# Performance work log

Hardware: AMD Instinct MI355X
Metric: run time of the kernel (lower is better)

The kernel has to match this reference:

```python
import jax, jax.numpy as jnp
import numpy as np

GAMMA = 0.9
TEMPERATURE = 0.07
BASE_TEMPERATURE = 0.07
U_SIZE = 15_000_000
BSZ, N_VIEWS, DIM = 2048, 2, 256


def setup_inputs() -> dict:
    key = jax.random.key(0)
    kf, = jax.random.split(key, 1)
    feats = jax.random.normal(kf, (BSZ, N_VIEWS, DIM), dtype=jnp.float32)
    # contrastive features are unit-normalized in practice
    feats = feats / jnp.linalg.norm(feats, axis=-1, keepdims=True)
    index = jnp.arange(BSZ, dtype=jnp.int64) if jax.config.jax_enable_x64 else jnp.arange(BSZ, dtype=jnp.int32)
    u = jnp.zeros((U_SIZE, 1), dtype=jnp.float32)
    return {"index": index, "features": feats, "u": u}


def reference(index, features, u):
    B, V, D = features.shape          # bsz, n_views, dim
    N = B * V
    eye_b = jnp.eye(B, dtype=jnp.float32)

    # torch.cat(torch.unbind(features, dim=1), dim=0) -> [V*B, D], views stacked
    contrast_feature = jnp.transpose(features, (1, 0, 2)).reshape(N, D)
    anchor_feature = contrast_feature  # contrast_mode == 'all'

    # [N, N] similarity logits
    anchor_dot_contrast = jnp.matmul(anchor_feature, contrast_feature.T) / TEMPERATURE
    logits_max = jax.lax.stop_gradient(jnp.max(anchor_dot_contrast, axis=1, keepdims=True))
    logits = anchor_dot_contrast - logits_max

    # positive mask: tiled identity with self-contrast removed
    mask = jnp.tile(eye_b, (V, V))
    logits_mask = 1.0 - jnp.eye(N, dtype=jnp.float32)  # scatter of zeros on the diagonal
    pos_mask = mask * logits_mask
    neg_mask = 1.0 - pos_mask

    # detached negative exp-logits (EMA statistics)
    neg_exp_logits = jax.lax.stop_gradient(jnp.exp(logits) * neg_mask)

    # indexed EMA buffer update: u[index] = (1-g)*u[index] + g*rowsum[:B]
    row_sum = jnp.sum(neg_exp_logits, axis=1, keepdims=True)[:B]   # [B, 1]
    u_new = (1.0 - GAMMA) * u[index] + GAMMA * row_sum             # [B, 1]
    # (buffer write: u = u.at[index].set(u_new); only u_new is read below)

    p_neg_pairs = neg_exp_logits / jnp.tile(u_new, (V, 1))         # [N, N], detached numer/denom
    log_prob = logits - jnp.sum(p_neg_pairs * logits * neg_mask, axis=1, keepdims=True)

    mean_log_prob_pos = jnp.sum(pos_mask * log_prob, axis=1) / jnp.sum(pos_mask, axis=1)
    loss = -(TEMPERATURE / BASE_TEMPERATURE) * mean_log_prob_pos
    return loss.reshape(V, B).mean()
```

## Files before the change

kernel.cpp:

```cpp
#include <hip/hip_runtime.h>


#define BSZ   2048
#define NROW  4096
#define DDIM  256
#define NB64  64
#define NT2   (NB64 * (NB64 + 1) / 2)
#define C1    (1.4426950408889634f / 0.07f)
#define LN2   0.6931471805599453f

typedef __attribute__((ext_vector_type(8))) __bf16 bf16x8;
typedef __attribute__((ext_vector_type(4))) float f32x4;

__device__ __forceinline__ short f2bs(float x) {
    __bf16 b = (__bf16)x;
    return __builtin_bit_cast(short, b);
}

__device__ __forceinline__ const float* crow_ptr(const float* feats, int i) {
    return feats + (((i & (BSZ - 1)) * 2 + (i >> 11)) << 8);
}

__global__ __launch_bounds__(256) void prep_kernel(const float* __restrict__ feats,
        float* __restrict__ msd, float* __restrict__ EWzero,
        short* __restrict__ CmF) {
    int tid = threadIdx.x;
    int z = blockIdx.x * 256 + tid;
    if (z < 2 * NROW) EWzero[z] = 0.0f;

    int lane = tid & 63;
    int row  = (blockIdx.x << 2) + (tid >> 6);
    const float4* src = (const float4*)crow_ptr(feats, row);
    float4 v = src[lane];
    float a0 = (float)(__bf16)v.x, a1 = (float)(__bf16)v.y;
    float a2 = (float)(__bf16)v.z, a3 = (float)(__bf16)v.w;
    float s = a0 * a0 + a1 * a1 + a2 * a2 + a3 * a3;
    #pragma unroll
    for (int off = 32; off; off >>= 1) s += __shfl_xor(s, off, 64);
    if (lane == 0) msd[row] = -s * C1;

    int gid  = z;
    int quad = gid & 3;
    int l15  = (gid >> 2) & 15;
    int rt   = (gid >> 6) & 3;
    int k    = (gid >> 8) & 7;
    int b    = gid >> 12;
    int srow = (b << 6) + (rt << 4) + l15;
    int kel  = (k << 5) + (quad << 3);
    const float4* fp = (const float4*)(crow_ptr(feats, srow) + kel);
    float4 v0 = fp[0], v1 = fp[1];
    short h[8] = { f2bs(v0.x), f2bs(v0.y), f2bs(v0.z), f2bs(v0.w),
                   f2bs(v1.x), f2bs(v1.y), f2bs(v1.z), f2bs(v1.w) };
    *(int4*)(CmF + gid * 8) = *(int4*)h;
}

__global__ __launch_bounds__(64, 2) void gemm_sym(const short* __restrict__ CmF,
        const float* __restrict__ msd, float* __restrict__ E,
        float* __restrict__ W2, float* __restrict__ Lpos) {
    int lane = threadIdx.x;
    int quad = lane >> 4;
    int l15  = lane & 15;

    int t = blockIdx.x;
    int p = (int)((sqrtf(8.0f * (float)t + 1.0f) - 1.0f) * 0.5f);
    while ((p + 1) * (p + 2) / 2 <= t) ++p;
    while (p * (p + 1) / 2 > t) --p;
    int q = t - p * (p + 1) / 2;
    int rowBase = q << 6;
    int colBase = p << 6;
    bool offdiag = (p != q);

    const short* aB = CmF + q * 16384 + ((l15 << 2) + quad) * 8;
    const short* bB = CmF + p * 16384 + ((l15 << 2) + quad) * 8;

    f32x4 acc[4][4];
    #pragma unroll
    for (int a = 0; a < 4; ++a)
        #pragma unroll
        for (int c = 0; c < 4; ++c) acc[a][c] = (f32x4){0.f, 0.f, 0.f, 0.f};

    bf16x8 aF[3][4], bF[3][4];
    #pragma unroll
    for (int rt = 0; rt < 4; ++rt) {
        aF[0][rt] = *(const bf16x8*)(aB + (0 * 4 + rt) * 512);
        bF[0][rt] = *(const bf16x8*)(bB + (0 * 4 + rt) * 512);
    }
    #pragma unroll
    for (int rt = 0; rt < 4; ++rt) {
        aF[1][rt] = *(const bf16x8*)(aB + (1 * 4 + rt) * 512);
        bF[1][rt] = *(const bf16x8*)(bB + (1 * 4 + rt) * 512);
    }

    #pragma unroll
    for (int k = 0; k < 8; ++k) {
        int cur = k % 3;
        int nxt = (k + 2) % 3;
        if (k < 6) {
            #pragma unroll
            for (int rt = 0; rt < 4; ++rt) {
                aF[nxt][rt] = *(const bf16x8*)(aB + ((k + 2) * 4 + rt) * 512);
                bF[nxt][rt] = *(const bf16x8*)(bB + ((k + 2) * 4 + rt) * 512);
            }
        }
        #pragma unroll
        for (int rt = 0; rt < 4; ++rt)
            #pragma unroll
            for (int ct = 0; ct < 4; ++ct)
                acc[rt][ct] = __builtin_amdgcn_mfma_f32_16x16x32_bf16(
                    aF[cur][rt], bF[cur][ct], acc[rt][ct], 0, 0, 0);
    }

    float msdr[4][4];
    #pragma unroll
    for (int rt = 0; rt < 4; ++rt)
        #pragma unroll
        for (int r = 0; r < 4; ++r)
            msdr[rt][r] = msd[rowBase + rt * 16 + (quad << 2) + r];
    float msdc[4];
    #pragma unroll
    for (int ct = 0; ct < 4; ++ct)
        msdc[ct] = msd[colBase + ct * 16 + l15];

    float Ep[4][4] = {}, Wp[4][4] = {};
    float Ec[4] = {}, Wc[4] = {};
    #pragma unroll
    for (int rt = 0; rt < 4; ++rt) {
        #pragma unroll
        for (int ct = 0; ct < 4; ++ct) {
            #pragma unroll
            for (int r = 0; r < 4; ++r) {
                float d = acc[rt][ct][r];
                float tt = __builtin_fmaf(d, C1, msdr[rt][r]);
                float e = __builtin_exp2f(tt);
                Ep[rt][r] += e;
                Wp[rt][r] = __builtin_fmaf(e, tt, Wp[rt][r]);
                if (offdiag) {
                    float t2 = __builtin_fmaf(d, C1, msdc[ct]);
                    float e2 = __builtin_exp2f(t2);
                    Ec[ct] += e2;
                    Wc[ct] = __builtin_fmaf(e2, t2, Wc[ct]);
                }
            }
        }
    }

    if (p == (q ^ 32)) {
        if (quad == (l15 >> 2)) {
            int r = l15 & 3;
            #pragma unroll
            for (int rt = 0; rt < 4; ++rt) {
                float d = acc[rt][rt][r];
                Lpos[rowBase + rt * 16 + l15] = __builtin_fmaf(d, C1, msdr[rt][r]);
                Lpos[colBase + rt * 16 + l15] = __builtin_fmaf(d, C1, msdc[rt]);
            }
        }
    }

    #pragma unroll
    for (int rt = 0; rt < 4; ++rt) {
        #pragma unroll
        for (int r = 0; r < 4; ++r) {
            float e = Ep[rt][r], w = Wp[rt][r];
            #pragma unroll
            for (int off = 1; off < 16; off <<= 1) {
                e += __shfl_xor(e, off, 64);
                w += __shfl_xor(w, off, 64);
            }
            if (l15 == 0) {
                int grow = rowBase + rt * 16 + (quad << 2) + r;
                atomicAdd(&E[grow], e);
                atomicAdd(&W2[grow], w);
            }
        }
    }
    if (offdiag) {
        #pragma unroll
        for (int ct = 0; ct < 4; ++ct) {
            float e = Ec[ct], w = Wc[ct];
            e += __shfl_xor(e, 16, 64);  w += __shfl_xor(w, 16, 64);
            e += __shfl_xor(e, 32, 64);  w += __shfl_xor(w, 32, 64);
            if (quad == 0) {
                int gcol = colBase + ct * 16 + l15;
                atomicAdd(&E[gcol], e);
                atomicAdd(&W2[gcol], w);
            }
        }
    }
}

__global__ __launch_bounds__(1024) void finalize_kernel(const int* __restrict__ index,
        const float* __restrict__ u, const float* __restrict__ E,
        const float* __restrict__ W2, const float* __restrict__ Lpos,
        float* __restrict__ out) {
    __shared__ float unew[BSZ];
    __shared__ float partial[16];
    int tid = threadIdx.x;
    for (int b = tid; b < BSZ; b += 1024) {
        float tp = Lpos[b];
        unew[b] = 0.1f * u[index[b]] + 0.9f * (E[b] - __builtin_exp2f(tp));
    }
    __syncthreads();
    float local = 0.0f;
    for (int i = tid; i < NROW; i += 1024) {
        float tp  = Lpos[i];
        float etp = __builtin_exp2f(tp);
        local += tp - (W2[i] - etp * tp) / unew[i & (BSZ - 1)];
    }
    #pragma unroll
    for (int off = 32; off; off >>= 1) local += __shfl_xor(local, off, 64);
    if ((tid & 63) == 0) partial[tid >> 6] = local;
    __syncthreads();
    if (tid == 0) {
        float s = 0.0f;
        #pragma unroll
        for (int w = 0; w < 16; ++w) s += partial[w];
        out[0] = -LN2 * s / (float)NROW;
    }
}

extern "C" void kernel_launch(void* const* d_in, const int* in_sizes, int n_in,
                              void* d_out, int out_size, void* d_ws, size_t ws_size,
                              hipStream_t stream) {
    const int*   index = (const int*)d_in[0];
    const float* feats = (const float*)d_in[1];
    const float* u     = (const float*)d_in[2];
    float* out = (float*)d_out;

    float* msd  = (float*)d_ws;
    float* E    = msd + NROW;
    float* W2   = E + NROW;
    float* Lpos = W2 + NROW;
    short* CmF  = (short*)((char*)d_ws + 131072);

    prep_kernel<<<1024, 256, 0, stream>>>(feats, msd, E, CmF);
    gemm_sym<<<NT2, 64, 0, stream>>>(CmF, msd, E, W2, Lpos);
    finalize_kernel<<<1, 1024, 0, stream>>>(index, u, E, W2, Lpos, out);
}
```

Baseline: 115.7 us.

## Factor row max out of exponent sums, sharing exp between row and column

Exponent sums are now computed without the per-row max shift, which is applied afterwards in finalize using the diagonal dot product. Off-diagonal tiles can then reuse one exp2 for both the row and the column accumulation, halving transcendental work in the epilogue, and the norm pass in prep is dropped. The prefetch pipeline goes from triple to double buffering, occupancy rises to 3 waves per SIMD, and MFMA sections get raised priority. Unshifted exponents rely on unit-normalized inputs (logits up to about 1/0.07) to stay within fp32 range.

```diff
diff --git a/kernel.cpp b/kernel.cpp
--- a/kernel.cpp
+++ b/kernel.cpp
@@ -22,24 +22,10 @@
 }
 
 __global__ __launch_bounds__(256) void prep_kernel(const float* __restrict__ feats,
-        float* __restrict__ msd, float* __restrict__ EWzero,
-        short* __restrict__ CmF) {
-    int tid = threadIdx.x;
-    int z = blockIdx.x * 256 + tid;
-    if (z < 2 * NROW) EWzero[z] = 0.0f;
-
-    int lane = tid & 63;
-    int row  = (blockIdx.x << 2) + (tid >> 6);
-    const float4* src = (const float4*)crow_ptr(feats, row);
-    float4 v = src[lane];
-    float a0 = (float)(__bf16)v.x, a1 = (float)(__bf16)v.y;
-    float a2 = (float)(__bf16)v.z, a3 = (float)(__bf16)v.w;
-    float s = a0 * a0 + a1 * a1 + a2 * a2 + a3 * a3;
-    #pragma unroll
-    for (int off = 32; off; off >>= 1) s += __shfl_xor(s, off, 64);
-    if (lane == 0) msd[row] = -s * C1;
-
-    int gid  = z;
+        float* __restrict__ Szero, short* __restrict__ CmF) {
+    int gid = blockIdx.x * 256 + threadIdx.x;
+    if (gid < 2 * NROW) Szero[gid] = 0.0f;
+
     int quad = gid & 3;
     int l15  = (gid >> 2) & 15;
     int rt   = (gid >> 6) & 3;
@@ -54,9 +40,9 @@
     *(int4*)(CmF + gid * 8) = *(int4*)h;
 }
 
-__global__ __launch_bounds__(64, 2) void gemm_sym(const short* __restrict__ CmF,
-        const float* __restrict__ msd, float* __restrict__ E,
-        float* __restrict__ W2, float* __restrict__ Lpos) {
+__global__ __launch_bounds__(64, 3) void gemm_sym(const short* __restrict__ CmF,
+        float* __restrict__ S1, float* __restrict__ S2,
+        float* __restrict__ Praw, float* __restrict__ Draw) {
     int lane = threadIdx.x;
     int quad = lane >> 4;
     int l15  = lane & 15;
@@ -70,8 +56,9 @@
     int colBase = p << 6;
     bool offdiag = (p != q);
 
-    const short* aB = CmF + q * 16384 + ((l15 << 2) + quad) * 8;
-    const short* bB = CmF + p * 16384 + ((l15 << 2) + quad) * 8;
+    int laneOff = ((l15 << 2) + quad) * 8;
+    int aO = q * 16384 + laneOff;
+    int bO = p * 16384 + laneOff;
 
     f32x4 acc[4][4];
     #pragma unroll
@@ -79,66 +66,50 @@
         #pragma unroll
         for (int c = 0; c < 4; ++c) acc[a][c] = (f32x4){0.f, 0.f, 0.f, 0.f};
 
-    bf16x8 aF[3][4], bF[3][4];
+    bf16x8 aF[2][4], bF[2][4];
     #pragma unroll
     for (int rt = 0; rt < 4; ++rt) {
-        aF[0][rt] = *(const bf16x8*)(aB + (0 * 4 + rt) * 512);
-        bF[0][rt] = *(const bf16x8*)(bB + (0 * 4 + rt) * 512);
-    }
-    #pragma unroll
-    for (int rt = 0; rt < 4; ++rt) {
-        aF[1][rt] = *(const bf16x8*)(aB + (1 * 4 + rt) * 512);
-        bF[1][rt] = *(const bf16x8*)(bB + (1 * 4 + rt) * 512);
+        aF[0][rt] = *(const bf16x8*)(CmF + aO + rt * 512);
+        bF[0][rt] = *(const bf16x8*)(CmF + bO + rt * 512);
     }
 
     #pragma unroll
     for (int k = 0; k < 8; ++k) {
-        int cur = k % 3;
-        int nxt = (k + 2) % 3;
-        if (k < 6) {
+        int cur = k & 1;
+        int nxt = cur ^ 1;
+        if (k < 7) {
             #pragma unroll
             for (int rt = 0; rt < 4; ++rt) {
-                aF[nxt][rt] = *(const bf16x8*)(aB + ((k + 2) * 4 + rt) * 512);
-                bF[nxt][rt] = *(const bf16x8*)(bB + ((k + 2) * 4 + rt) * 512);
-            }
-        }
+                aF[nxt][rt] = *(const bf16x8*)(CmF + aO + ((k + 1) * 4 + rt) * 512);
+                bF[nxt][rt] = *(const bf16x8*)(CmF + bO + ((k + 1) * 4 + rt) * 512);
+            }
+        }
+        __builtin_amdgcn_s_setprio(1);
         #pragma unroll
         for (int rt = 0; rt < 4; ++rt)
             #pragma unroll
             for (int ct = 0; ct < 4; ++ct)
                 acc[rt][ct] = __builtin_amdgcn_mfma_f32_16x16x32_bf16(
                     aF[cur][rt], bF[cur][ct], acc[rt][ct], 0, 0, 0);
-    }
-
-    float msdr[4][4];
-    #pragma unroll
-    for (int rt = 0; rt < 4; ++rt)
-        #pragma unroll
-        for (int r = 0; r < 4; ++r)
-            msdr[rt][r] = msd[rowBase + rt * 16 + (quad << 2) + r];
-    float msdc[4];
-    #pragma unroll
-    for (int ct = 0; ct < 4; ++ct)
-        msdc[ct] = msd[colBase + ct * 16 + l15];
-
-    float Ep[4][4] = {}, Wp[4][4] = {};
-    float Ec[4] = {}, Wc[4] = {};
+        __builtin_amdgcn_s_setprio(0);
+    }
+
+    float S1r[4][4] = {}, S2r[4][4] = {};
+    float S1c[4] = {}, S2c[4] = {};
     #pragma unroll
     for (int rt = 0; rt < 4; ++rt) {
         #pragma unroll
         for (int ct = 0; ct < 4; ++ct) {
             #pragma unroll
             for (int r = 0; r < 4; ++r) {
-                float d = acc[rt][ct][r];
-                float tt = __builtin_fmaf(d, C1, msdr[rt][r]);
-                float e = __builtin_exp2f(tt);
-                Ep[rt][r] += e;
-                Wp[rt][r] = __builtin_fmaf(e, tt, Wp[rt][r]);
+                float d  = acc[rt][ct][r];
+                float t0 = d * C1;
+                float f  = __builtin_exp2f(t0);
+                S1r[rt][r] += f;
+                S2r[rt][r] = __builtin_fmaf(f, t0, S2r[rt][r]);
                 if (offdiag) {
-                    float t2 = __builtin_fmaf(d, C1, msdc[ct]);
-                    float e2 = __builtin_exp2f(t2);
-                    Ec[ct] += e2;
-                    Wc[ct] = __builtin_fmaf(e2, t2, Wc[ct]);
+                    S1c[ct] += f;
+                    S2c[ct] = __builtin_fmaf(f, t0, S2c[ct]);
                 }
             }
         }
@@ -149,10 +120,18 @@
             int r = l15 & 3;
             #pragma unroll
             for (int rt = 0; rt < 4; ++rt) {
-                float d = acc[rt][rt][r];
-                Lpos[rowBase + rt * 16 + l15] = __builtin_fmaf(d, C1, msdr[rt][r]);
-                Lpos[colBase + rt * 16 + l15] = __builtin_fmaf(d, C1, msdc[rt]);
-            }
+                float t0 = acc[rt][rt][r] * C1;
+                Praw[rowBase + rt * 16 + l15] = t0;
+                Praw[colBase + rt * 16 + l15] = t0;
+            }
+        }
+    }
+    if (!offdiag) {
+        if (quad == (l15 >> 2)) {
+            int r = l15 & 3;
+            #pragma unroll
+            for (int rt = 0; rt < 4; ++rt)
+                Draw[rowBase + rt * 16 + l15] = acc[rt][rt][r] * C1;
         }
     }
 
@@ -160,7 +139,7 @@
     for (int rt = 0; rt < 4; ++rt) {
         #pragma unroll
         for (int r = 0; r < 4; ++r) {
-            float e = Ep[rt][r], w = Wp[rt][r];
+            float e = S1r[rt][r], w = S2r[rt][r];
             #pragma unroll
             for (int off = 1; off < 16; off <<= 1) {
                 e += __shfl_xor(e, off, 64);
@@ -168,43 +147,47 @@
             }
             if (l15 == 0) {
                 int grow = rowBase + rt * 16 + (quad << 2) + r;
-                atomicAdd(&E[grow], e);
-                atomicAdd(&W2[grow], w);
+                atomicAdd(&S1[grow], e);
+                atomicAdd(&S2[grow], w);
             }
         }
     }
     if (offdiag) {
         #pragma unroll
         for (int ct = 0; ct < 4; ++ct) {
-            float e = Ec[ct], w = Wc[ct];
+            float e = S1c[ct], w = S2c[ct];
             e += __shfl_xor(e, 16, 64);  w += __shfl_xor(w, 16, 64);
             e += __shfl_xor(e, 32, 64);  w += __shfl_xor(w, 32, 64);
             if (quad == 0) {
                 int gcol = colBase + ct * 16 + l15;
-                atomicAdd(&E[gcol], e);
-                atomicAdd(&W2[gcol], w);
+                atomicAdd(&S1[gcol], e);
+                atomicAdd(&S2[gcol], w);
             }
         }
     }
 }
 
 __global__ __launch_bounds__(1024) void finalize_kernel(const int* __restrict__ index,
-        const float* __restrict__ u, const float* __restrict__ E,
-        const float* __restrict__ W2, const float* __restrict__ Lpos,
-        float* __restrict__ out) {
+        const float* __restrict__ u, const float* __restrict__ S1,
+        const float* __restrict__ S2, const float* __restrict__ Praw,
+        const float* __restrict__ Draw, float* __restrict__ out) {
     __shared__ float unew[BSZ];
     __shared__ float partial[16];
     int tid = threadIdx.x;
     for (int b = tid; b < BSZ; b += 1024) {
-        float tp = Lpos[b];
-        unew[b] = 0.1f * u[index[b]] + 0.9f * (E[b] - __builtin_exp2f(tp));
+        float m  = -Draw[b];
+        float tp = Praw[b] + m;
+        float E  = __builtin_exp2f(m) * S1[b];
+        unew[b] = 0.1f * u[index[b]] + 0.9f * (E - __builtin_exp2f(tp));
     }
     __syncthreads();
     float local = 0.0f;
     for (int i = tid; i < NROW; i += 1024) {
-        float tp  = Lpos[i];
+        float m   = -Draw[i];
+        float tp  = Praw[i] + m;
         float etp = __builtin_exp2f(tp);
-        local += tp - (W2[i] - etp * tp) / unew[i & (BSZ - 1)];
+        float W   = __builtin_exp2f(m) * __builtin_fmaf(m, S1[i], S2[i]);
+        local += tp - (W - etp * tp) / unew[i & (BSZ - 1)];
     }
     #pragma unroll
     for (int off = 32; off; off >>= 1) local += __shfl_xor(local, off, 64);
@@ -226,13 +209,13 @@
     const float* u     = (const float*)d_in[2];
     float* out = (float*)d_out;
 
-    float* msd  = (float*)d_ws;
-    float* E    = msd + NROW;
-    float* W2   = E + NROW;
-    float* Lpos = W2 + NROW;
+    float* S1   = (float*)d_ws;
+    float* S2   = S1 + NROW;
+    float* Praw = S2 + NROW;
+    float* Draw = Praw + NROW;
     short* CmF  = (short*)((char*)d_ws + 131072);
 
-    prep_kernel<<<1024, 256, 0, stream>>>(feats, msd, E, CmF);
-    gemm_sym<<<NT2, 64, 0, stream>>>(CmF, msd, E, W2, Lpos);
-    finalize_kernel<<<1, 1024, 0, stream>>>(index, u, E, W2, Lpos, out);
-}
+    prep_kernel<<<1024, 256, 0, stream>>>(feats, S1, CmF);
+    gemm_sym<<<NT2, 64, 0, stream>>>(CmF, S1, S2, Praw, Draw);
+    finalize_kernel<<<1, 1024, 0, stream>>>(index, u, S1, S2, Praw, Draw, out);
+}
```

New measurement: 114.2 us. Within noise of the previous version (-1.3%).
